# Kernel tuning notes

Measured on AMD Instinct MI355X. Metric: run time of the kernel, lower is better.

The kernel has to match this reference:

```python
import jax, jax.numpy as jnp
import numpy as np

G = 4
EPS = 1e-5

def group_norm(x, gamma, beta):
    B, C, D, H, W = x.shape
    xg = x.reshape(B, G, C // G, D, H, W)
    mu = xg.mean(axis=(2, 3, 4, 5), keepdims=True)
    var = xg.var(axis=(2, 3, 4, 5), keepdims=True)
    xn = ((xg - mu) * jax.lax.rsqrt(var + EPS)).reshape(B, C, D, H, W)
    return xn * gamma[None, :, None, None, None] + beta[None, :, None, None, None]

def conv3d(x, w, b):
    y = jax.lax.conv_general_dilated(x, w, (1, 1, 1), [(1, 1), (1, 1), (1, 1)],
                                     dimension_numbers=('NCDHW', 'OIDHW', 'NCDHW'))
    return y + b[None, :, None, None, None]

def deform_conv_hw(x, offset, w, b):
    # x: [B,C,D,H,W]; offset: [B, 2*27, D,H,W] -> per-tap (dh, dw); depth taps are rigid.
    B, C, D, H, W = x.shape
    off = offset.reshape(B, 27, 2, D, H, W)
    xp = jnp.pad(x, ((0, 0), (0, 0), (1, 1), (0, 0), (0, 0)))  # zero-pad depth only
    hh = jnp.arange(H, dtype=x.dtype)[None, None, :, None]
    ww = jnp.arange(W, dtype=x.dtype)[None, None, None, :]
    bi = jnp.arange(B)[:, None, None, None]
    di = jnp.arange(D)[None, :, None, None]
    out = jnp.zeros((B, w.shape[0], D, H, W), x.dtype)
    tap = 0
    for i in range(3):
        x_d = xp[:, :, i:i + D]  # depth-shifted view [B,C,D,H,W]
        for j in range(3):
            for k in range(3):
                hp = hh + (j - 1) + off[:, tap, 0]  # [B,D,H,W] fractional h position
                wp = ww + (k - 1) + off[:, tap, 1]
                h0 = jnp.floor(hp); w0 = jnp.floor(wp)
                h0i = h0.astype(jnp.int32); w0i = w0.astype(jnp.int32)
                lh = hp - h0; lw = wp - w0
                def gather(hi, wi):
                    m = ((hi >= 0) & (hi < H) & (wi >= 0) & (wi < W)).astype(x.dtype)
                    g = x_d[bi, :, di, jnp.clip(hi, 0, H - 1), jnp.clip(wi, 0, W - 1)]  # [B,D,H,W,C]
                    return g, m
                g00, m00 = gather(h0i, w0i)
                g01, m01 = gather(h0i, w0i + 1)
                g10, m10 = gather(h0i + 1, w0i)
                g11, m11 = gather(h0i + 1, w0i + 1)
                val = (((1 - lh) * (1 - lw) * m00)[..., None] * g00
                       + ((1 - lh) * lw * m01)[..., None] * g01
                       + (lh * (1 - lw) * m10)[..., None] * g10
                       + (lh * lw * m11)[..., None] * g11)
                out = out + jnp.einsum('bdhwc,oc->bodhw', val, w[:, :, i, j, k])
                tap += 1
    return out + b[None, :, None, None, None]

def setup_inputs():
    key = jax.random.key(0)
    ks = jax.random.split(key, 8)
    B, C, D, H, W = 1, 32, 24, 96, 96
    x = jax.random.normal(ks[0], (B, C, D, H, W), jnp.float32)
    g1 = jnp.ones((C,), jnp.float32); be1 = jnp.zeros((C,), jnp.float32)
    g2 = jnp.ones((C,), jnp.float32); be2 = jnp.zeros((C,), jnp.float32)
    ow1 = jax.random.normal(ks[1], (54, C, 3, 3, 3), jnp.float32) * 0.02
    ob1 = jnp.zeros((54,), jnp.float32)
    dw1 = jax.random.normal(ks[2], (C, C, 3, 3, 3), jnp.float32) * 0.05
    db1 = jnp.zeros((C,), jnp.float32)
    ow2 = jax.random.normal(ks[3], (54, C, 3, 3, 3), jnp.float32) * 0.02
    ob2 = jnp.zeros((54,), jnp.float32)
    dw2 = jax.random.normal(ks[4], (C, C, 3, 3, 3), jnp.float32) * 0.05
    db2 = jnp.zeros((C,), jnp.float32)
    return {"x": x, "g1": g1, "be1": be1, "g2": g2, "be2": be2,
            "ow1": ow1, "ob1": ob1, "dw1": dw1, "db1": db1,
            "ow2": ow2, "ob2": ob2, "dw2": dw2, "db2": db2}

def reference(x, g1, be1, g2, be2, ow1, ob1, dw1, db1, ow2, ob2, dw2, db2):
    h = jax.nn.relu(group_norm(x, g1, be1))
    h = deform_conv_hw(h, conv3d(h, ow1, ob1), dw1, db1)
    h = jax.nn.relu(group_norm(h, g2, be2))
    h = deform_conv_hw(h, conv3d(h, ow2, ob2), dw2, db2)
    return h + x
```

## Files before the change

kernel.cpp:

```cpp
#include <hip/hip_runtime.h>
#include <hip/hip_fp16.h>

#define CC   32
#define DD   24
#define HH   96
#define WW   96
#define HWC  (HH*WW)
#define DHW  (DD*HH*WW)
#define NG   4
#define CPG  (CC/NG)
#define OC1  54
#define GN_EPS 1e-5f

#define NBLK_F (DHW/128)
#define CHUNK_F (NBLK_F/8)
#define NBLK_G (DHW/256)
#define CHUNK_G (NBLK_G/8)

typedef float  f32x4 __attribute__((ext_vector_type(4)));
typedef _Float16 f16x8 __attribute__((ext_vector_type(8)));
typedef unsigned int u32x4 __attribute__((ext_vector_type(4)));

union F16Frag { f16x8 v; __half2 h2[4]; };

__device__ __forceinline__ int swz(int bid, int chunk) {
    return (bid % 8) * chunk + (bid / 8);
}

__global__ void pack_w(const float* __restrict__ src, _Float16* __restrict__ dst,
                       int O, int NT, int n) {
    int idx = blockIdx.x * 256 + threadIdx.x;
    if (idx >= n) return;
    int e    = idx & 7;
    int lane = (idx >> 3) & 63;
    int nt   = (idx >> 9) % NT;
    int tap  = (idx >> 9) / NT;
    int o = nt * 16 + (lane & 15);
    int c = (lane >> 4) * 8 + e;
    float v = (o < O) ? src[(o * CC + c) * 27 + tap] : 0.f;
    dst[idx] = (_Float16)v;
}

__global__ void gn_stats(const float* __restrict__ x, float* __restrict__ stats) {
    const int g = blockIdx.x >> 5;
    const int s = blockIdx.x & 31;
    const float4* base = (const float4*)(x + (size_t)g * CPG * DHW);
    const int n4 = CPG * DHW / 4;
    float s1 = 0.f, s2 = 0.f;
    for (int idx = s * 256 + threadIdx.x; idx < n4; idx += 32 * 256) {
        float4 v = base[idx];
        s1 += v.x + v.y + v.z + v.w;
        s2 += v.x * v.x + v.y * v.y + v.z * v.z + v.w * v.w;
    }
    for (int off = 32; off > 0; off >>= 1) {
        s1 += __shfl_down(s1, off);
        s2 += __shfl_down(s2, off);
    }
    __shared__ float ls1[4], ls2[4];
    int wid = threadIdx.x >> 6;
    if ((threadIdx.x & 63) == 0) { ls1[wid] = s1; ls2[wid] = s2; }
    __syncthreads();
    if (threadIdx.x == 0) {
        float a = 0.f, b = 0.f;
        for (int i = 0; i < 4; i++) { a += ls1[i]; b += ls2[i]; }
        atomicAdd(&stats[g * 2 + 0], a);
        atomicAdd(&stats[g * 2 + 1], b);
    }
}

__global__ void gn_apply_T(const float* __restrict__ x, const float* __restrict__ stats,
                           const float* __restrict__ gamma, const float* __restrict__ beta,
                           __half* __restrict__ yT) {
    const int p = swz(blockIdx.x, CHUNK_G) * 256 + threadIdx.x;
    const float invN = 1.0f / (float)(CPG * DHW);
    float mean[NG], rstd[NG];
#pragma unroll
    for (int g = 0; g < NG; g++) {
        mean[g] = stats[2 * g] * invN;
        float var = stats[2 * g + 1] * invN - mean[g] * mean[g];
        rstd[g] = rsqrtf(var + GN_EPS);
    }
    float vals[CC];
#pragma unroll
    for (int c = 0; c < CC; c++) {
        const int g = c >> 3;
        const float ga = gamma[c] * rstd[g];
        const float be = beta[c] - mean[g] * ga;
        vals[c] = fmaxf(0.f, x[(size_t)c * DHW + p] * ga + be);
    }
    union { __half2 h2[16]; u32x4 q[4]; } u;
#pragma unroll
    for (int c = 0; c < 16; c++) u.h2[c] = __floats2half2_rn(vals[2 * c], vals[2 * c + 1]);
    u32x4* dst = (u32x4*)(yT + (size_t)p * CC);
#pragma unroll
    for (int q = 0; q < 4; q++) dst[q] = u.q[q];
}

#define OPAD 70
__global__ __launch_bounds__(128, 3) void fused_conv(const __half* __restrict__ xT,
                                                     const _Float16* __restrict__ wBo,
                                                     const float* __restrict__ ob,
                                                     const _Float16* __restrict__ wBd,
                                                     const float* __restrict__ db,
                                                     const float* __restrict__ resid,
                                                     float* __restrict__ outp) {
    __shared__ __align__(16) char lds_raw[CC * 132 * 4];
    __half* offs_lds = (__half*)lds_raw;
    float*  out_lds  = (float*)lds_raw;

    const int tid  = threadIdx.x;
    const int lane = tid & 63;
    const int wave = tid >> 6;
    const int p0   = swz(blockIdx.x, CHUNK_F) * 128;
    const int pw   = p0 + wave * 64;
    const int d    = pw / HWC;
    const int rem  = pw % HWC;
    const int mrow = lane & 15;
    const int kg   = lane >> 4;
    const int wbase = wave * (OC1 * OPAD);

    int hq[4], wq[4];
#pragma unroll
    for (int m = 0; m < 4; m++) {
        int rr = rem + m * 16 + mrow;
        hq[m] = rr / WW; wq[m] = rr % WW;
    }

    f32x4 aco[4][4];
#pragma unroll
    for (int m = 0; m < 4; m++)
#pragma unroll
        for (int n = 0; n < 4; n++) aco[m][n] = (f32x4){0.f, 0.f, 0.f, 0.f};

    const f16x8* wbo8 = (const f16x8*)wBo;

#pragma unroll 1
    for (int i = 0; i < 3; i++) {
        const int dd = d + i - 1;
        if ((unsigned)dd >= DD) continue;
        const __half* xd = xT + (size_t)dd * HWC * CC;
#pragma unroll 3
        for (int jk = 0; jk < 9; jk++) {
            const int j = jk / 3, k = jk % 3, tap = i * 9 + jk;
            const f16x8 b0 = wbo8[(tap * 4 + 0) * 64 + lane];
            const f16x8 b1 = wbo8[(tap * 4 + 1) * 64 + lane];
            const f16x8 b2 = wbo8[(tap * 4 + 2) * 64 + lane];
            const f16x8 b3 = wbo8[(tap * 4 + 3) * 64 + lane];
            f16x8 a[4];
#pragma unroll
            for (int m = 0; m < 4; m++) {
                const int hh = hq[m] + j - 1;
                const int ww = wq[m] + k - 1;
                a[m] = (f16x8){0, 0, 0, 0, 0, 0, 0, 0};
                if ((unsigned)hh < HH && (unsigned)ww < WW)
                    a[m] = *(const f16x8*)(xd + (size_t)(hh * WW + ww) * CC + kg * 8);
            }
#pragma unroll
            for (int m = 0; m < 4; m++) {
                aco[m][0] = __builtin_amdgcn_mfma_f32_16x16x32_f16(a[m], b0, aco[m][0], 0, 0, 0);
                aco[m][1] = __builtin_amdgcn_mfma_f32_16x16x32_f16(a[m], b1, aco[m][1], 0, 0, 0);
                aco[m][2] = __builtin_amdgcn_mfma_f32_16x16x32_f16(a[m], b2, aco[m][2], 0, 0, 0);
                aco[m][3] = __builtin_amdgcn_mfma_f32_16x16x32_f16(a[m], b3, aco[m][3], 0, 0, 0);
            }
        }
    }

    float bo[4];
#pragma unroll
    for (int nt = 0; nt < 4; nt++) {
        const int o = nt * 16 + mrow;
        bo[nt] = (o < OC1) ? ob[o] : 0.f;
    }
#pragma unroll
    for (int m = 0; m < 4; m++) {
#pragma unroll
        for (int nt = 0; nt < 4; nt++) {
            const int o = nt * 16 + mrow;
            if (o < OC1) {
                const int idx = wbase + o * OPAD + m * 16 + kg * 4;
                __half2 lo = __floats2half2_rn(aco[m][nt].x + bo[nt], aco[m][nt].y + bo[nt]);
                __half2 hi = __floats2half2_rn(aco[m][nt].z + bo[nt], aco[m][nt].w + bo[nt]);
                *(__half2*)&offs_lds[idx]     = lo;
                *(__half2*)&offs_lds[idx + 2] = hi;
            }
        }
    }
    __syncthreads();

    f32x4 acd[4][2];
#pragma unroll
    for (int m = 0; m < 4; m++) {
        acd[m][0] = (f32x4){0.f, 0.f, 0.f, 0.f};
        acd[m][1] = (f32x4){0.f, 0.f, 0.f, 0.f};
    }

    const f16x8* wbd8 = (const f16x8*)wBd;

#pragma unroll 1
    for (int i = 0; i < 3; i++) {
        const int dd = d + i - 1;
        if ((unsigned)dd >= DD) continue;
        const __half* xd = xT + (size_t)dd * HWC * CC;
#pragma unroll 1
        for (int jk = 0; jk < 9; jk++) {
            const int j = jk / 3, k = jk % 3, tap = i * 9 + jk;
            const f16x8 b0 = wbd8[(tap * 2 + 0) * 64 + lane];
            const f16x8 b1 = wbd8[(tap * 2 + 1) * 64 + lane];
            int i00[4], i01[4], i10[4], i11[4];
            float c00[4], c01[4], c10[4], c11[4];
#pragma unroll
            for (int m = 0; m < 4; m++) {
                const int ptl = m * 16 + mrow;
                const float oh = __half2float(offs_lds[wbase + (2 * tap + 0) * OPAD + ptl]);
                const float ov = __half2float(offs_lds[wbase + (2 * tap + 1) * OPAD + ptl]);
                const float hp  = (float)(hq[m] + j - 1) + oh;
                const float wpf = (float)(wq[m] + k - 1) + ov;
                const float h0f = floorf(hp), w0f = floorf(wpf);
                const int h0 = (int)h0f, w0 = (int)w0f;
                const float lh = hp - h0f, lw = wpf - w0f;
                const bool hv0 = (h0 >= 0) && (h0 < HH);
                const bool hv1 = (h0 >= -1) && (h0 < HH - 1);
                const bool wv0 = (w0 >= 0) && (w0 < WW);
                const bool wv1 = (w0 >= -1) && (w0 < WW - 1);
                c00[m] = (hv0 && wv0) ? (1.f - lh) * (1.f - lw) : 0.f;
                c01[m] = (hv0 && wv1) ? (1.f - lh) * lw : 0.f;
                c10[m] = (hv1 && wv0) ? lh * (1.f - lw) : 0.f;
                c11[m] = (hv1 && wv1) ? lh * lw : 0.f;
                const int h0c = min(max(h0, 0), HH - 1);
                const int h1c = min(max(h0 + 1, 0), HH - 1);
                const int w0c = min(max(w0, 0), WW - 1);
                const int w1c = min(max(w0 + 1, 0), WW - 1);
                i00[m] = h0c * WW + w0c;
                i01[m] = h0c * WW + w1c;
                i10[m] = h1c * WW + w0c;
                i11[m] = h1c * WW + w1c;
            }
#pragma unroll
            for (int m = 0; m < 4; m++) {
                F16Frag a00, a01, a10, a11, A;
                a00.v = *(const f16x8*)(xd + (size_t)i00[m] * CC + kg * 8);
                a01.v = *(const f16x8*)(xd + (size_t)i01[m] * CC + kg * 8);
                a10.v = *(const f16x8*)(xd + (size_t)i10[m] * CC + kg * 8);
                a11.v = *(const f16x8*)(xd + (size_t)i11[m] * CC + kg * 8);
                const __half2 C00 = __float2half2_rn(c00[m]);
                const __half2 C01 = __float2half2_rn(c01[m]);
                const __half2 C10 = __float2half2_rn(c10[m]);
                const __half2 C11 = __float2half2_rn(c11[m]);
#pragma unroll
                for (int r = 0; r < 4; r++) {
                    __half2 t = __hmul2(C00, a00.h2[r]);
                    t = __hfma2(C01, a01.h2[r], t);
                    t = __hfma2(C10, a10.h2[r], t);
                    t = __hfma2(C11, a11.h2[r], t);
                    A.h2[r] = t;
                }
                acd[m][0] = __builtin_amdgcn_mfma_f32_16x16x32_f16(A.v, b0, acd[m][0], 0, 0, 0);
                acd[m][1] = __builtin_amdgcn_mfma_f32_16x16x32_f16(A.v, b1, acd[m][1], 0, 0, 0);
            }
        }
    }
    __syncthreads();

#pragma unroll
    for (int m = 0; m < 4; m++)
#pragma unroll
        for (int nt = 0; nt < 2; nt++) {
            const int o = nt * 16 + mrow;
            *(f32x4*)&out_lds[o * 132 + wave * 64 + m * 16 + kg * 4] = acd[m][nt];
        }
    __syncthreads();
    if (resid) {
#pragma unroll 1
        for (int o = 0; o < CC; o++) {
            float v = out_lds[o * 132 + tid] + db[o] + resid[(size_t)o * DHW + p0 + tid];
            outp[(size_t)o * DHW + p0 + tid] = v;
        }
    } else {
#pragma unroll 1
        for (int o = 0; o < CC; o++)
            outp[(size_t)o * DHW + p0 + tid] = out_lds[o * 132 + tid] + db[o];
    }
}

extern "C" void kernel_launch(void* const* d_in, const int* in_sizes, int n_in,
                              void* d_out, int out_size, void* d_ws, size_t ws_size,
                              hipStream_t stream) {
    const float* x   = (const float*)d_in[0];
    const float* g1  = (const float*)d_in[1];
    const float* be1 = (const float*)d_in[2];
    const float* g2  = (const float*)d_in[3];
    const float* be2 = (const float*)d_in[4];
    const float* ow1 = (const float*)d_in[5];
    const float* ob1 = (const float*)d_in[6];
    const float* dw1 = (const float*)d_in[7];
    const float* db1 = (const float*)d_in[8];
    const float* ow2 = (const float*)d_in[9];
    const float* ob2 = (const float*)d_in[10];
    const float* dw2 = (const float*)d_in[11];
    const float* db2 = (const float*)d_in[12];
    float* out = (float*)d_out;
    float* ws  = (float*)d_ws;

    float*    stats = ws;
    _Float16* wBo1  = (_Float16*)(ws + 256);
    _Float16* wBd1  = (_Float16*)(ws + 27904);
    _Float16* wBo2  = (_Float16*)(ws + 41728);
    _Float16* wBd2  = (_Float16*)(ws + 69376);
    __half*   hT    = (__half*)(ws + 83200);

    (void)hipMemsetAsync(stats, 0, 16 * sizeof(float), stream);
    pack_w<<<(27 * 4 * 512 + 255) / 256, 256, 0, stream>>>(ow1, wBo1, 54, 4, 27 * 4 * 512);
    pack_w<<<(27 * 2 * 512 + 255) / 256, 256, 0, stream>>>(dw1, wBd1, 32, 2, 27 * 2 * 512);
    pack_w<<<(27 * 4 * 512 + 255) / 256, 256, 0, stream>>>(ow2, wBo2, 54, 4, 27 * 4 * 512);
    pack_w<<<(27 * 2 * 512 + 255) / 256, 256, 0, stream>>>(dw2, wBd2, 32, 2, 27 * 2 * 512);

    gn_stats<<<NG * 32, 256, 0, stream>>>(x, stats + 0);
    gn_apply_T<<<NBLK_G, 256, 0, stream>>>(x, stats + 0, g1, be1, hT);
    fused_conv<<<NBLK_F, 128, 0, stream>>>(hT, wBo1, ob1, wBd1, db1, nullptr, out);

    gn_stats<<<NG * 32, 256, 0, stream>>>(out, stats + 8);
    gn_apply_T<<<NBLK_G, 256, 0, stream>>>(out, stats + 8, g2, be2, hT);
    fused_conv<<<NBLK_F, 128, 0, stream>>>(hT, wBo2, ob2, wBd2, db2, x, out);
}
```

Baseline: 367.4 us.

## Pad activation buffer spatially and halve conv tile to raise occupancy

The transposed fp16 activation buffer gets a one-pixel zero halo in H and W (98x98 planes), cleared by a memset each call. This removes the bounds checks and predicated loads from the offset-conv gather. The fused conv kernel now handles 64 points per block instead of 128 (two M-tiles per wave), with launch bounds raised to 6 blocks per SM, smaller LDS and a deform loop unrolled by 3. This is meant to raise occupancy and latency hiding for the gathers, at the cost of an extra memset of about 15 MB and reloading the weights across twice as many blocks.

```diff
diff --git a/kernel.cpp b/kernel.cpp
--- a/kernel.cpp
+++ b/kernel.cpp
@@ -12,7 +12,11 @@
 #define OC1  54
 #define GN_EPS 1e-5f
 
-#define NBLK_F (DHW/128)
+#define WP   98
+#define PLP  (WP*WP)
+#define NHP  (DD*PLP*CC)
+
+#define NBLK_F (DHW/64)
 #define CHUNK_F (NBLK_F/8)
 #define NBLK_G (DHW/256)
 #define CHUNK_G (NBLK_G/8)
@@ -70,7 +74,7 @@
 
 __global__ void gn_apply_T(const float* __restrict__ x, const float* __restrict__ stats,
                            const float* __restrict__ gamma, const float* __restrict__ beta,
-                           __half* __restrict__ yT) {
+                           __half* __restrict__ yTp) {
     const int p = swz(blockIdx.x, CHUNK_G) * 256 + threadIdx.x;
     const float invN = 1.0f / (float)(CPG * DHW);
     float mean[NG], rstd[NG];
@@ -91,44 +95,48 @@
     union { __half2 h2[16]; u32x4 q[4]; } u;
 #pragma unroll
     for (int c = 0; c < 16; c++) u.h2[c] = __floats2half2_rn(vals[2 * c], vals[2 * c + 1]);
-    u32x4* dst = (u32x4*)(yT + (size_t)p * CC);
+    const int d = p / HWC;
+    const int rr = p % HWC;
+    const int h = rr / WW;
+    const int w = rr % WW;
+    u32x4* dst = (u32x4*)(yTp + ((size_t)d * PLP + (size_t)(h + 1) * WP + (w + 1)) * CC);
 #pragma unroll
     for (int q = 0; q < 4; q++) dst[q] = u.q[q];
 }
 
-#define OPAD 70
-__global__ __launch_bounds__(128, 3) void fused_conv(const __half* __restrict__ xT,
+#define OPAD 34
+__global__ __launch_bounds__(128, 6) void fused_conv(const __half* __restrict__ xTp,
                                                      const _Float16* __restrict__ wBo,
                                                      const float* __restrict__ ob,
                                                      const _Float16* __restrict__ wBd,
                                                      const float* __restrict__ db,
                                                      const float* __restrict__ resid,
                                                      float* __restrict__ outp) {
-    __shared__ __align__(16) char lds_raw[CC * 132 * 4];
+    __shared__ __align__(16) char lds_raw[CC * 68 * 4];
     __half* offs_lds = (__half*)lds_raw;
     float*  out_lds  = (float*)lds_raw;
 
     const int tid  = threadIdx.x;
     const int lane = tid & 63;
     const int wave = tid >> 6;
-    const int p0   = swz(blockIdx.x, CHUNK_F) * 128;
-    const int pw   = p0 + wave * 64;
+    const int p0   = swz(blockIdx.x, CHUNK_F) * 64;
+    const int pw   = p0 + wave * 32;
     const int d    = pw / HWC;
     const int rem  = pw % HWC;
     const int mrow = lane & 15;
     const int kg   = lane >> 4;
     const int wbase = wave * (OC1 * OPAD);
 
-    int hq[4], wq[4];
-#pragma unroll
-    for (int m = 0; m < 4; m++) {
+    int hq[2], wq[2];
+#pragma unroll
+    for (int m = 0; m < 2; m++) {
         int rr = rem + m * 16 + mrow;
         hq[m] = rr / WW; wq[m] = rr % WW;
     }
 
-    f32x4 aco[4][4];
-#pragma unroll
-    for (int m = 0; m < 4; m++)
+    f32x4 aco[2][4];
+#pragma unroll
+    for (int m = 0; m < 2; m++)
 #pragma unroll
         for (int n = 0; n < 4; n++) aco[m][n] = (f32x4){0.f, 0.f, 0.f, 0.f};
 
@@ -138,7 +146,7 @@
     for (int i = 0; i < 3; i++) {
         const int dd = d + i - 1;
         if ((unsigned)dd >= DD) continue;
-        const __half* xd = xT + (size_t)dd * HWC * CC;
+        const __half* xd = xTp + (size_t)dd * PLP * CC;
 #pragma unroll 3
         for (int jk = 0; jk < 9; jk++) {
             const int j = jk / 3, k = jk % 3, tap = i * 9 + jk;
@@ -146,17 +154,12 @@
             const f16x8 b1 = wbo8[(tap * 4 + 1) * 64 + lane];
             const f16x8 b2 = wbo8[(tap * 4 + 2) * 64 + lane];
             const f16x8 b3 = wbo8[(tap * 4 + 3) * 64 + lane];
-            f16x8 a[4];
-#pragma unroll
-            for (int m = 0; m < 4; m++) {
-                const int hh = hq[m] + j - 1;
-                const int ww = wq[m] + k - 1;
-                a[m] = (f16x8){0, 0, 0, 0, 0, 0, 0, 0};
-                if ((unsigned)hh < HH && (unsigned)ww < WW)
-                    a[m] = *(const f16x8*)(xd + (size_t)(hh * WW + ww) * CC + kg * 8);
-            }
-#pragma unroll
-            for (int m = 0; m < 4; m++) {
+            f16x8 a[2];
+#pragma unroll
+            for (int m = 0; m < 2; m++)
+                a[m] = *(const f16x8*)(xd + (size_t)((hq[m] + j) * WP + wq[m] + k) * CC + kg * 8);
+#pragma unroll
+            for (int m = 0; m < 2; m++) {
                 aco[m][0] = __builtin_amdgcn_mfma_f32_16x16x32_f16(a[m], b0, aco[m][0], 0, 0, 0);
                 aco[m][1] = __builtin_amdgcn_mfma_f32_16x16x32_f16(a[m], b1, aco[m][1], 0, 0, 0);
                 aco[m][2] = __builtin_amdgcn_mfma_f32_16x16x32_f16(a[m], b2, aco[m][2], 0, 0, 0);
@@ -172,7 +175,7 @@
         bo[nt] = (o < OC1) ? ob[o] : 0.f;
     }
 #pragma unroll
-    for (int m = 0; m < 4; m++) {
+    for (int m = 0; m < 2; m++) {
 #pragma unroll
         for (int nt = 0; nt < 4; nt++) {
             const int o = nt * 16 + mrow;
@@ -187,9 +190,9 @@
     }
     __syncthreads();
 
-    f32x4 acd[4][2];
-#pragma unroll
-    for (int m = 0; m < 4; m++) {
+    f32x4 acd[2][2];
+#pragma unroll
+    for (int m = 0; m < 2; m++) {
         acd[m][0] = (f32x4){0.f, 0.f, 0.f, 0.f};
         acd[m][1] = (f32x4){0.f, 0.f, 0.f, 0.f};
     }
@@ -200,16 +203,16 @@
     for (int i = 0; i < 3; i++) {
         const int dd = d + i - 1;
         if ((unsigned)dd >= DD) continue;
-        const __half* xd = xT + (size_t)dd * HWC * CC;
-#pragma unroll 1
+        const __half* xd = xTp + (size_t)dd * PLP * CC;
+#pragma unroll 3
         for (int jk = 0; jk < 9; jk++) {
             const int j = jk / 3, k = jk % 3, tap = i * 9 + jk;
             const f16x8 b0 = wbd8[(tap * 2 + 0) * 64 + lane];
             const f16x8 b1 = wbd8[(tap * 2 + 1) * 64 + lane];
-            int i00[4], i01[4], i10[4], i11[4];
-            float c00[4], c01[4], c10[4], c11[4];
-#pragma unroll
-            for (int m = 0; m < 4; m++) {
+            int i00[2], i01[2], i10[2], i11[2];
+            float c00[2], c01[2], c10[2], c11[2];
+#pragma unroll
+            for (int m = 0; m < 2; m++) {
                 const int ptl = m * 16 + mrow;
                 const float oh = __half2float(offs_lds[wbase + (2 * tap + 0) * OPAD + ptl]);
                 const float ov = __half2float(offs_lds[wbase + (2 * tap + 1) * OPAD + ptl]);
@@ -226,17 +229,17 @@
                 c01[m] = (hv0 && wv1) ? (1.f - lh) * lw : 0.f;
                 c10[m] = (hv1 && wv0) ? lh * (1.f - lw) : 0.f;
                 c11[m] = (hv1 && wv1) ? lh * lw : 0.f;
-                const int h0c = min(max(h0, 0), HH - 1);
-                const int h1c = min(max(h0 + 1, 0), HH - 1);
-                const int w0c = min(max(w0, 0), WW - 1);
-                const int w1c = min(max(w0 + 1, 0), WW - 1);
-                i00[m] = h0c * WW + w0c;
-                i01[m] = h0c * WW + w1c;
-                i10[m] = h1c * WW + w0c;
-                i11[m] = h1c * WW + w1c;
+                const int h0c = min(max(h0, 0), HH - 1) + 1;
+                const int h1c = min(max(h0 + 1, 0), HH - 1) + 1;
+                const int w0c = min(max(w0, 0), WW - 1) + 1;
+                const int w1c = min(max(w0 + 1, 0), WW - 1) + 1;
+                i00[m] = h0c * WP + w0c;
+                i01[m] = h0c * WP + w1c;
+                i10[m] = h1c * WP + w0c;
+                i11[m] = h1c * WP + w1c;
             }
 #pragma unroll
-            for (int m = 0; m < 4; m++) {
+            for (int m = 0; m < 2; m++) {
                 F16Frag a00, a01, a10, a11, A;
                 a00.v = *(const f16x8*)(xd + (size_t)i00[m] * CC + kg * 8);
                 a01.v = *(const f16x8*)(xd + (size_t)i01[m] * CC + kg * 8);
@@ -262,23 +265,28 @@
     __syncthreads();
 
 #pragma unroll
-    for (int m = 0; m < 4; m++)
+    for (int m = 0; m < 2; m++)
 #pragma unroll
         for (int nt = 0; nt < 2; nt++) {
             const int o = nt * 16 + mrow;
-            *(f32x4*)&out_lds[o * 132 + wave * 64 + m * 16 + kg * 4] = acd[m][nt];
+            *(f32x4*)&out_lds[o * 68 + wave * 32 + m * 16 + kg * 4] = acd[m][nt];
         }
     __syncthreads();
+    const int pp = tid & 63;
+    const int obh = tid >> 6;
     if (resid) {
-#pragma unroll 1
-        for (int o = 0; o < CC; o++) {
-            float v = out_lds[o * 132 + tid] + db[o] + resid[(size_t)o * DHW + p0 + tid];
-            outp[(size_t)o * DHW + p0 + tid] = v;
+#pragma unroll
+        for (int o2 = 0; o2 < 16; o2++) {
+            const int o = o2 * 2 + obh;
+            float v = out_lds[o * 68 + pp] + db[o] + resid[(size_t)o * DHW + p0 + pp];
+            outp[(size_t)o * DHW + p0 + pp] = v;
         }
     } else {
-#pragma unroll 1
-        for (int o = 0; o < CC; o++)
-            outp[(size_t)o * DHW + p0 + tid] = out_lds[o * 132 + tid] + db[o];
+#pragma unroll
+        for (int o2 = 0; o2 < 16; o2++) {
+            const int o = o2 * 2 + obh;
+            outp[(size_t)o * DHW + p0 + pp] = out_lds[o * 68 + pp] + db[o];
+        }
     }
 }
 
@@ -306,19 +314,20 @@
     _Float16* wBd1  = (_Float16*)(ws + 27904);
     _Float16* wBo2  = (_Float16*)(ws + 41728);
     _Float16* wBd2  = (_Float16*)(ws + 69376);
-    __half*   hT    = (__half*)(ws + 83200);
+    __half*   hTp   = (__half*)(ws + 83200);
 
     (void)hipMemsetAsync(stats, 0, 16 * sizeof(float), stream);
+    (void)hipMemsetAsync(hTp, 0, (size_t)NHP * sizeof(__half), stream);
     pack_w<<<(27 * 4 * 512 + 255) / 256, 256, 0, stream>>>(ow1, wBo1, 54, 4, 27 * 4 * 512);
     pack_w<<<(27 * 2 * 512 + 255) / 256, 256, 0, stream>>>(dw1, wBd1, 32, 2, 27 * 2 * 512);
     pack_w<<<(27 * 4 * 512 + 255) / 256, 256, 0, stream>>>(ow2, wBo2, 54, 4, 27 * 4 * 512);
     pack_w<<<(27 * 2 * 512 + 255) / 256, 256, 0, stream>>>(dw2, wBd2, 32, 2, 27 * 2 * 512);
 
     gn_stats<<<NG * 32, 256, 0, stream>>>(x, stats + 0);
-    gn_apply_T<<<NBLK_G, 256, 0, stream>>>(x, stats + 0, g1, be1, hT);
-    fused_conv<<<NBLK_F, 128, 0, stream>>>(hT, wBo1, ob1, wBd1, db1, nullptr, out);
+    gn_apply_T<<<NBLK_G, 256, 0, stream>>>(x, stats + 0, g1, be1, hTp);
+    fused_conv<<<NBLK_F, 128, 0, stream>>>(hTp, wBo1, ob1, wBd1, db1, nullptr, out);
 
     gn_stats<<<NG * 32, 256, 0, stream>>>(out, stats + 8);
-    gn_apply_T<<<NBLK_G, 256, 0, stream>>>(out, stats + 8, g2, be2, hT);
-    fused_conv<<<NBLK_F, 128, 0, stream>>>(hT, wBo2, ob2, wBd2, db2, x, out);
-}
+    gn_apply_T<<<NBLK_G, 256, 0, stream>>>(out, stats + 8, g2, be2, hTp);
+    fused_conv<<<NBLK_F, 128, 0, stream>>>(hTp, wBo2, ob2, wBd2, db2, x, out);
+}
```

New measurement: 450.7 us. 1.23x slower.

## Store normalized activations in zero-padded halo layout to drop bounds checks

Applied to the files above, without the earlier changes.

The normalized fp16 activation buffer is now stored with a one-pixel zero halo in H and W (98x98 planes), cleared by a memset. The regular offset conv loads without bounds tests. The deformable sampler takes a wave-uniform fast path that reads four adjacent neighbours from a single base pointer when every lane is in range, and falls back to clamped sampling otherwise. A block barrier after the offset write to LDS is also removed, relying on each wave only reading its own region. The cost is an extra memset of about 15 MB and a larger buffer.

```diff
diff --git a/kernel.cpp b/kernel.cpp
--- a/kernel.cpp
+++ b/kernel.cpp
@@ -11,6 +11,10 @@
 #define CPG  (CC/NG)
 #define OC1  54
 #define GN_EPS 1e-5f
+
+#define WP   98
+#define PLP  (WP*WP)
+#define NHP  (DD*PLP*CC)
 
 #define NBLK_F (DHW/128)
 #define CHUNK_F (NBLK_F/8)
@@ -70,7 +74,7 @@
 
 __global__ void gn_apply_T(const float* __restrict__ x, const float* __restrict__ stats,
                            const float* __restrict__ gamma, const float* __restrict__ beta,
-                           __half* __restrict__ yT) {
+                           __half* __restrict__ yTp) {
     const int p = swz(blockIdx.x, CHUNK_G) * 256 + threadIdx.x;
     const float invN = 1.0f / (float)(CPG * DHW);
     float mean[NG], rstd[NG];
@@ -91,13 +95,17 @@
     union { __half2 h2[16]; u32x4 q[4]; } u;
 #pragma unroll
     for (int c = 0; c < 16; c++) u.h2[c] = __floats2half2_rn(vals[2 * c], vals[2 * c + 1]);
-    u32x4* dst = (u32x4*)(yT + (size_t)p * CC);
+    const int d = p / HWC;
+    const int rr = p % HWC;
+    const int h = rr / WW;
+    const int w = rr % WW;
+    u32x4* dst = (u32x4*)(yTp + ((size_t)d * PLP + (size_t)(h + 1) * WP + (w + 1)) * CC);
 #pragma unroll
     for (int q = 0; q < 4; q++) dst[q] = u.q[q];
 }
 
 #define OPAD 70
-__global__ __launch_bounds__(128, 3) void fused_conv(const __half* __restrict__ xT,
+__global__ __launch_bounds__(128, 3) void fused_conv(const __half* __restrict__ xTp,
                                                      const _Float16* __restrict__ wBo,
                                                      const float* __restrict__ ob,
                                                      const _Float16* __restrict__ wBd,
@@ -138,7 +146,7 @@
     for (int i = 0; i < 3; i++) {
         const int dd = d + i - 1;
         if ((unsigned)dd >= DD) continue;
-        const __half* xd = xT + (size_t)dd * HWC * CC;
+        const __half* xd = xTp + (size_t)dd * PLP * CC;
 #pragma unroll 3
         for (int jk = 0; jk < 9; jk++) {
             const int j = jk / 3, k = jk % 3, tap = i * 9 + jk;
@@ -148,13 +156,8 @@
             const f16x8 b3 = wbo8[(tap * 4 + 3) * 64 + lane];
             f16x8 a[4];
 #pragma unroll
-            for (int m = 0; m < 4; m++) {
-                const int hh = hq[m] + j - 1;
-                const int ww = wq[m] + k - 1;
-                a[m] = (f16x8){0, 0, 0, 0, 0, 0, 0, 0};
-                if ((unsigned)hh < HH && (unsigned)ww < WW)
-                    a[m] = *(const f16x8*)(xd + (size_t)(hh * WW + ww) * CC + kg * 8);
-            }
+            for (int m = 0; m < 4; m++)
+                a[m] = *(const f16x8*)(xd + (size_t)((hq[m] + j) * WP + wq[m] + k) * CC + kg * 8);
 #pragma unroll
             for (int m = 0; m < 4; m++) {
                 aco[m][0] = __builtin_amdgcn_mfma_f32_16x16x32_f16(a[m], b0, aco[m][0], 0, 0, 0);
@@ -185,7 +188,6 @@
             }
         }
     }
-    __syncthreads();
 
     f32x4 acd[4][2];
 #pragma unroll
@@ -200,14 +202,12 @@
     for (int i = 0; i < 3; i++) {
         const int dd = d + i - 1;
         if ((unsigned)dd >= DD) continue;
-        const __half* xd = xT + (size_t)dd * HWC * CC;
+        const __half* xd = xTp + (size_t)dd * PLP * CC;
 #pragma unroll 1
         for (int jk = 0; jk < 9; jk++) {
             const int j = jk / 3, k = jk % 3, tap = i * 9 + jk;
             const f16x8 b0 = wbd8[(tap * 2 + 0) * 64 + lane];
             const f16x8 b1 = wbd8[(tap * 2 + 1) * 64 + lane];
-            int i00[4], i01[4], i10[4], i11[4];
-            float c00[4], c01[4], c10[4], c11[4];
 #pragma unroll
             for (int m = 0; m < 4; m++) {
                 const int ptl = m * 16 + mrow;
@@ -216,36 +216,44 @@
                 const float hp  = (float)(hq[m] + j - 1) + oh;
                 const float wpf = (float)(wq[m] + k - 1) + ov;
                 const float h0f = floorf(hp), w0f = floorf(wpf);
-                const int h0 = (int)h0f, w0 = (int)w0f;
+                const int h0p = (int)h0f + 1;
+                const int w0p = (int)w0f + 1;
                 const float lh = hp - h0f, lw = wpf - w0f;
-                const bool hv0 = (h0 >= 0) && (h0 < HH);
-                const bool hv1 = (h0 >= -1) && (h0 < HH - 1);
-                const bool wv0 = (w0 >= 0) && (w0 < WW);
-                const bool wv1 = (w0 >= -1) && (w0 < WW - 1);
-                c00[m] = (hv0 && wv0) ? (1.f - lh) * (1.f - lw) : 0.f;
-                c01[m] = (hv0 && wv1) ? (1.f - lh) * lw : 0.f;
-                c10[m] = (hv1 && wv0) ? lh * (1.f - lw) : 0.f;
-                c11[m] = (hv1 && wv1) ? lh * lw : 0.f;
-                const int h0c = min(max(h0, 0), HH - 1);
-                const int h1c = min(max(h0 + 1, 0), HH - 1);
-                const int w0c = min(max(w0, 0), WW - 1);
-                const int w1c = min(max(w0 + 1, 0), WW - 1);
-                i00[m] = h0c * WW + w0c;
-                i01[m] = h0c * WW + w1c;
-                i10[m] = h1c * WW + w0c;
-                i11[m] = h1c * WW + w1c;
-            }
-#pragma unroll
-            for (int m = 0; m < 4; m++) {
                 F16Frag a00, a01, a10, a11, A;
-                a00.v = *(const f16x8*)(xd + (size_t)i00[m] * CC + kg * 8);
-                a01.v = *(const f16x8*)(xd + (size_t)i01[m] * CC + kg * 8);
-                a10.v = *(const f16x8*)(xd + (size_t)i10[m] * CC + kg * 8);
-                a11.v = *(const f16x8*)(xd + (size_t)i11[m] * CC + kg * 8);
-                const __half2 C00 = __float2half2_rn(c00[m]);
-                const __half2 C01 = __float2half2_rn(c01[m]);
-                const __half2 C10 = __float2half2_rn(c10[m]);
-                const __half2 C11 = __float2half2_rn(c11[m]);
+                float c00, c01, c10, c11;
+                if (__all((unsigned)h0p <= (unsigned)HH && (unsigned)w0p <= (unsigned)WW)) {
+                    const __half* g = xd + (size_t)(h0p * WP + w0p) * CC + kg * 8;
+                    a00.v = *(const f16x8*)g;
+                    a01.v = *(const f16x8*)(g + CC);
+                    a10.v = *(const f16x8*)(g + WP * CC);
+                    a11.v = *(const f16x8*)(g + WP * CC + CC);
+                    c00 = (1.f - lh) * (1.f - lw);
+                    c01 = (1.f - lh) * lw;
+                    c10 = lh * (1.f - lw);
+                    c11 = lh * lw;
+                } else {
+                    const int h0 = h0p - 1, w0 = w0p - 1;
+                    const bool hv0 = (h0 >= 0) && (h0 < HH);
+                    const bool hv1 = (h0 >= -1) && (h0 < HH - 1);
+                    const bool wv0 = (w0 >= 0) && (w0 < WW);
+                    const bool wv1 = (w0 >= -1) && (w0 < WW - 1);
+                    c00 = (hv0 && wv0) ? (1.f - lh) * (1.f - lw) : 0.f;
+                    c01 = (hv0 && wv1) ? (1.f - lh) * lw : 0.f;
+                    c10 = (hv1 && wv0) ? lh * (1.f - lw) : 0.f;
+                    c11 = (hv1 && wv1) ? lh * lw : 0.f;
+                    const int h0c = min(max(h0, 0), HH - 1) + 1;
+                    const int h1c = min(max(h0 + 1, 0), HH - 1) + 1;
+                    const int w0c = min(max(w0, 0), WW - 1) + 1;
+                    const int w1c = min(max(w0 + 1, 0), WW - 1) + 1;
+                    a00.v = *(const f16x8*)(xd + (size_t)(h0c * WP + w0c) * CC + kg * 8);
+                    a01.v = *(const f16x8*)(xd + (size_t)(h0c * WP + w1c) * CC + kg * 8);
+                    a10.v = *(const f16x8*)(xd + (size_t)(h1c * WP + w0c) * CC + kg * 8);
+                    a11.v = *(const f16x8*)(xd + (size_t)(h1c * WP + w1c) * CC + kg * 8);
+                }
+                const __half2 C00 = __float2half2_rn(c00);
+                const __half2 C01 = __float2half2_rn(c01);
+                const __half2 C10 = __float2half2_rn(c10);
+                const __half2 C11 = __float2half2_rn(c11);
 #pragma unroll
                 for (int r = 0; r < 4; r++) {
                     __half2 t = __hmul2(C00, a00.h2[r]);
@@ -306,19 +314,20 @@
     _Float16* wBd1  = (_Float16*)(ws + 27904);
     _Float16* wBo2  = (_Float16*)(ws + 41728);
     _Float16* wBd2  = (_Float16*)(ws + 69376);
-    __half*   hT    = (__half*)(ws + 83200);
+    __half*   hTp   = (__half*)(ws + 83200);
 
     (void)hipMemsetAsync(stats, 0, 16 * sizeof(float), stream);
+    (void)hipMemsetAsync(hTp, 0, (size_t)NHP * sizeof(__half), stream);
     pack_w<<<(27 * 4 * 512 + 255) / 256, 256, 0, stream>>>(ow1, wBo1, 54, 4, 27 * 4 * 512);
     pack_w<<<(27 * 2 * 512 + 255) / 256, 256, 0, stream>>>(dw1, wBd1, 32, 2, 27 * 2 * 512);
     pack_w<<<(27 * 4 * 512 + 255) / 256, 256, 0, stream>>>(ow2, wBo2, 54, 4, 27 * 4 * 512);
     pack_w<<<(27 * 2 * 512 + 255) / 256, 256, 0, stream>>>(dw2, wBd2, 32, 2, 27 * 2 * 512);
 
     gn_stats<<<NG * 32, 256, 0, stream>>>(x, stats + 0);
-    gn_apply_T<<<NBLK_G, 256, 0, stream>>>(x, stats + 0, g1, be1, hT);
-    fused_conv<<<NBLK_F, 128, 0, stream>>>(hT, wBo1, ob1, wBd1, db1, nullptr, out);
+    gn_apply_T<<<NBLK_G, 256, 0, stream>>>(x, stats + 0, g1, be1, hTp);
+    fused_conv<<<NBLK_F, 128, 0, stream>>>(hTp, wBo1, ob1, wBd1, db1, nullptr, out);
 
     gn_stats<<<NG * 32, 256, 0, stream>>>(out, stats + 8);
-    gn_apply_T<<<NBLK_G, 256, 0, stream>>>(out, stats + 8, g2, be2, hT);
-    fused_conv<<<NBLK_F, 128, 0, stream>>>(hT, wBo2, ob2, wBd2, db2, x, out);
-}
+    gn_apply_T<<<NBLK_G, 256, 0, stream>>>(out, stats + 8, g2, be2, hTp);
+    fused_conv<<<NBLK_F, 128, 0, stream>>>(hTp, wBo2, ob2, wBd2, db2, x, out);
+}
```

Result: slower. 430.5 us (+17.1%).
